# Optimization experiments

Measured on AMD Instinct MI355X. Metric: run time of the kernel, lower is better.

## Reference

```python
import jax, jax.numpy as jnp
import numpy as np

N, E, G = 50000, 800000, 64
IN, HID, H, C, OUT = 4, 128, 2, 64, 7  # HID = heads*C = 128
EPS = 1e-5
NEG_SLOPE = 0.2


def setup_inputs() -> dict:
    key = jax.random.key(0)
    ks = jax.random.split(key, 24)
    rn = lambda k, shape, s=0.1: (jax.random.normal(k, shape, jnp.float32) * s)
    inp = {
        "x": jax.random.normal(ks[0], (N, IN), jnp.float32),
        "edge_index": jax.random.randint(ks[1], (2, E), 0, N, jnp.int64),
        "batch": jnp.sort(jax.random.randint(ks[2], (N,), 0, G, jnp.int64)),
        # GATv2 layer 1: lin_l (source), lin_r (target), attention vector, bias
        "Wl1": rn(ks[3], (IN, HID)), "Wr1": rn(ks[4], (IN, HID)),
        "att1": rn(ks[5], (H, C)), "b1": rn(ks[6], (HID,)),
        "g1": jnp.ones((HID,), jnp.float32), "be1": jnp.zeros((HID,), jnp.float32),
        # GATv2 layer 2
        "Wl2": rn(ks[7], (HID, HID)), "Wr2": rn(ks[8], (HID, HID)),
        "att2": rn(ks[9], (H, C)), "b2": rn(ks[10], (HID,)),
        "g2": jnp.ones((HID,), jnp.float32), "be2": jnp.zeros((HID,), jnp.float32),
        # MLP head
        "W3": rn(ks[11], (HID, C)), "b3": rn(ks[12], (C,)),
        "W4": rn(ks[13], (C, OUT)), "b4": rn(ks[14], (OUT,)),
    }
    return inp


def gatv2_conv(x, src, dst, Wl, Wr, att, bias):
    """PyG GATv2Conv, heads=H, concat=True, self-loops already in (src,dst)."""
    n = x.shape[0]
    xl = (x @ Wl).reshape(n, H, C)  # source-side transform
    xr = (x @ Wr).reshape(n, H, C)  # target-side transform
    m = xl[src] + xr[dst]                                   # [E', H, C]
    e = jnp.einsum('ehc,hc->eh', jax.nn.leaky_relu(m, NEG_SLOPE), att)
    # segment softmax over edges sharing a destination node
    emax = jax.ops.segment_max(e, dst, num_segments=n)
    p = jnp.exp(e - emax[dst])
    denom = jax.ops.segment_sum(p, dst, num_segments=n)
    alpha = p / denom[dst]                                  # [E', H]
    out = jax.ops.segment_sum(alpha[..., None] * xl[src], dst, num_segments=n)
    return out.reshape(n, H * C) + bias


def batchnorm(x, gamma, beta):
    mu = jnp.mean(x, axis=0)
    var = jnp.mean(jnp.square(x - mu), axis=0)  # biased var (torch train norm)
    return gamma * (x - mu) * jax.lax.rsqrt(var + EPS) + beta


def reference(x, edge_index, batch, Wl1, Wr1, att1, b1, g1, be1,
              Wl2, Wr2, att2, b2, g2, be2, W3, b3, W4, b4):
    n = x.shape[0]
    loops = jnp.arange(n, dtype=edge_index.dtype)
    src = jnp.concatenate([edge_index[0], loops])
    dst = jnp.concatenate([edge_index[1], loops])

    h = jax.nn.relu(batchnorm(gatv2_conv(x, src, dst, Wl1, Wr1, att1, b1), g1, be1))
    h = jax.nn.relu(batchnorm(gatv2_conv(h, src, dst, Wl2, Wr2, att2, b2), g2, be2))

    # global mean pool over graphs
    sums = jax.ops.segment_sum(h, batch, num_segments=G)
    cnts = jax.ops.segment_sum(jnp.ones((n, 1), h.dtype), batch, num_segments=G)
    pooled = sums / jnp.maximum(cnts, 1.0)

    out = jax.nn.relu(pooled @ W3 + b3)
    return out @ W4 + b4
```

## Files before the change

kernel.cpp:

```cpp
#include <hip/hip_runtime.h>
#include <hip/hip_bf16.h>

typedef __hip_bfloat16 bf16;
typedef unsigned short u16;
typedef unsigned int u32;
typedef long long i64;
typedef short bf16x8 __attribute__((ext_vector_type(8)));
typedef float f32x4 __attribute__((ext_vector_type(4)));

#define N_NODES 50000
#define E_EDGES 800000
#define G_GRAPHS 64
#define HID 128
#define OUT_F 7
#define EPSBN 1e-5f
#define NEG 0.2f
#define NB_G 2048
#define SCAN_B 196
#define PB_NODES 32
#define XP 136
#define NXF 25000
#define NEB 3125
#define NB_X 1024
#define NTILES 3125

__device__ __forceinline__ float b2f(bf16 v) { return __bfloat162float(v); }
__device__ __forceinline__ float ldf(const void* p, int i, int fm) {
    return fm ? ((const float*)p)[i] : b2f(((const bf16*)p)[i]);
}
__device__ __forceinline__ int ldi(const void* p, i64 i, int im) {
    return im ? (int)((const i64*)p)[i] : ((const int*)p)[i];
}
__device__ __forceinline__ void stf(void* p, int i, int fm, float v) {
    if (fm) ((float*)p)[i] = v; else ((bf16*)p)[i] = __float2bfloat16(v);
}
__device__ __forceinline__ float bl(u32 u) { return __uint_as_float(u << 16); }
__device__ __forceinline__ float bh(u32 u) { return __uint_as_float(u & 0xFFFF0000u); }

template <int CTRL>
__device__ __forceinline__ float dpp_add(float t) {
    int v = __builtin_amdgcn_update_dpp(0, __float_as_int(t), CTRL, 0xF, 0xF, true);
    return t + __int_as_float(v);
}

__global__ void k_init(const void* __restrict__ x, const void* __restrict__ ei,
                       int* __restrict__ flags,
                       float* __restrict__ z1, int n1, float* __restrict__ z2, int n2) {
    int t = threadIdx.x;
    if (blockIdx.x == 0) {
        __shared__ int sh[2];
        if (t == 0) { sh[0] = 0; sh[1] = 1; }
        __syncthreads();
        const u16* xb = (const u16*)x;
        int huge = 0;
        for (int i = t; i < 1024; i += 256) {
            int e = (xb[i] >> 7) & 0xFF;
            if (e >= 0x90) huge = 1;
        }
        if (huge) atomicOr(&sh[0], 1);
        const u32* eb = (const u32*)ei;
        int nz = 0;
        for (int i = t; i < 512; i += 256)
            if (eb[2 * i + 1] != 0) nz = 1;
        if (nz) atomicAnd(&sh[1], 0);
        __syncthreads();
        if (t == 0) { flags[0] = sh[0]; flags[1] = sh[1]; }
    } else {
        int i = (blockIdx.x - 1) * 256 + t;
        int stride = (gridDim.x - 1) * 256;
        for (; i < n1 + n2; i += stride) {
            if (i < n1) z1[i] = 0.0f;
            else z2[i - n1] = 0.0f;
        }
    }
}

__global__ void k_deg(const void* __restrict__ ei, const int* __restrict__ flags,
                      int* __restrict__ deg) {
    int im = flags[1];
    int e = blockIdx.x * 256 + threadIdx.x;
    if (e >= E_EDGES) return;
    int d = ldi(ei, (i64)E_EDGES + e, im);
    atomicAdd(&deg[d], 1);
}

__global__ void k_scan1(const int* __restrict__ deg, int* __restrict__ bsum) {
    __shared__ int s[256];
    int t = threadIdx.x, i = blockIdx.x * 256 + t;
    s[t] = (i < N_NODES) ? deg[i] : 0;
    __syncthreads();
    for (int off = 128; off > 0; off >>= 1) {
        if (t < off) s[t] += s[t + off];
        __syncthreads();
    }
    if (t == 0) bsum[blockIdx.x] = s[0];
}

__global__ void k_scan2(int* __restrict__ bsum) {
    __shared__ int s[256];
    int t = threadIdx.x;
    int orig = (t < SCAN_B) ? bsum[t] : 0;
    s[t] = orig;
    __syncthreads();
    for (int off = 1; off < 256; off <<= 1) {
        int v = (t >= off) ? s[t - off] : 0;
        __syncthreads();
        s[t] += v;
        __syncthreads();
    }
    if (t < SCAN_B) bsum[t] = s[t] - orig;
}

__global__ void k_scan3(const int* __restrict__ deg, const int* __restrict__ bsum,
                        int* __restrict__ rowptr, int* __restrict__ cursor) {
    __shared__ int s[256];
    int t = threadIdx.x, i = blockIdx.x * 256 + t;
    int v = (i < N_NODES) ? deg[i] : 0;
    s[t] = v;
    __syncthreads();
    for (int off = 1; off < 256; off <<= 1) {
        int a = (t >= off) ? s[t - off] : 0;
        __syncthreads();
        s[t] += a;
        __syncthreads();
    }
    int excl = s[t] - v + bsum[blockIdx.x];
    if (i < N_NODES) { rowptr[i] = excl; cursor[i] = excl; }
    if (i == N_NODES - 1) rowptr[N_NODES] = excl + v;
}

__global__ __launch_bounds__(256) void k_fillprep(
    const void* __restrict__ ei, int* __restrict__ cursor, u16* __restrict__ csr,
    const void* __restrict__ x, const void* __restrict__ Wl, const void* __restrict__ Wr,
    const void* __restrict__ Wl2, const void* __restrict__ Wr2,
    const int* __restrict__ flags,
    bf16* __restrict__ xl, bf16* __restrict__ xr, bf16* __restrict__ WT) {
    int b = blockIdx.x;
    if (b < NEB) {
        int im = flags[1];
        int e = b * 256 + threadIdx.x;
        if (e < E_EDGES) {
            int src = ldi(ei, e, im);
            int d   = ldi(ei, (i64)E_EDGES + e, im);
            int pos = atomicAdd(&cursor[d], 1);
            csr[pos] = (u16)src;
        }
    } else if (b < NEB + NXF) {
        int fm = flags[0];
        int idx = (b - NEB) * 256 + threadIdx.x;
        int n = idx >> 7, j = idx & 127;
        float a = 0.f, bb = 0.f;
#pragma unroll
        for (int k = 0; k < 4; k++) {
            float xv = ldf(x, n * 4 + k, fm);
            a += xv * ldf(Wl, k * HID + j, fm);
            bb += xv * ldf(Wr, k * HID + j, fm);
        }
        xl[idx] = __float2bfloat16(a);
        xr[idx] = __float2bfloat16(bb);
    } else {
        int fm = flags[0];
        int idx = (b - NEB - NXF) * 256 + threadIdx.x;
        int mat = idx >> 14, r = idx & 16383, j = r >> 7, k = r & 127;
        const void* W = mat ? Wr2 : Wl2;
        WT[idx] = __float2bfloat16(ldf(W, k * HID + j, fm));
    }
}

__global__ __launch_bounds__(256) void k_gather(
    const bf16* __restrict__ XLp, const bf16* __restrict__ XRp,
    const void* __restrict__ att, const void* __restrict__ bias,
    const int* __restrict__ rowptr, const u16* __restrict__ csr,
    const int* __restrict__ flags,
    float* __restrict__ A, float* __restrict__ partial) {
    __shared__ float ls[128], lq[128];
    int t = threadIdx.x;
    if (t < 128) { ls[t] = 0.f; lq[t] = 0.f; }
    __syncthreads();
    int fm = flags[0];
    int lane = t & 63, waveid = t >> 6;
    int half = lane >> 5;
    int headq = (lane >> 4) & 1;
    int c16 = lane & 15;
    int cbase = headq * 64 + c16 * 4;
    const u32* XLw = (const u32*)XLp;
    const u32* XRw = (const u32*)XRp;
    u32 coff = (u32)(cbase >> 1);
    float a0 = ldf(att, cbase + 0, fm), a1 = ldf(att, cbase + 1, fm);
    float a2 = ldf(att, cbase + 2, fm), a3 = ldf(att, cbase + 3, fm);
    float bb0 = ldf(bias, cbase + 0, fm), bb1 = ldf(bias, cbase + 1, fm);
    float bb2 = ldf(bias, cbase + 2, fm), bb3 = ldf(bias, cbase + 3, fm);
    float s0 = 0, s1 = 0, s2 = 0, s3 = 0, q0 = 0, q1 = 0, q2 = 0, q3 = 0;

    for (int d = blockIdx.x * 4 + waveid; d < N_NODES; d += NB_G * 4) {
        int rp = rowptr[d];
        int deg = rowptr[d + 1] - rp;
        int count = deg + 1;
        u32 roff = ((u32)d << 6) + coff;
        u32 r01 = XRw[roff], r23 = XRw[roff + 1];
        float xr0 = bl(r01), xr1 = bh(r01), xr2 = bl(r23), xr3 = bh(r23);
        float acc0 = 0, acc1 = 0, acc2 = 0, acc3 = 0, den = 0;
        int sA = d; if (half < deg) sA = (int)csr[rp + half];
        int sB = d; if (2 + half < deg) sB = (int)csr[rp + 2 + half];
        u32 offA = ((u32)sA << 6) + coff;
        u32 a01 = XLw[offA], a23 = XLw[offA + 1];
        u32 offB = ((u32)sB << 6) + coff;
        u32 b01 = XLw[offB], b23 = XLw[offB + 1];
        int sC = d; if (4 + half < deg) sC = (int)csr[rp + 4 + half];
        int sD = d; if (6 + half < deg) sD = (int)csr[rp + 6 + half];
        for (int i = 0; i < count; i += 4) {
            u32 offC = ((u32)sC << 6) + coff;
            u32 n01 = XLw[offC], n23 = XLw[offC + 1];
            u32 offD = ((u32)sD << 6) + coff;
            u32 m01 = XLw[offD], m23 = XLw[offD + 1];
            int eE = i + 8 + half, eF = i + 10 + half;
            int sE = d; if (eE < deg) sE = (int)csr[rp + eE];
            int sF = d; if (eF < deg) sF = (int)csr[rp + eF];
            {
                float x0 = bl(a01), x1 = bh(a01), x2 = bl(a23), x3 = bh(a23);
                float m0 = x0 + xr0, m1 = x1 + xr1, m2 = x2 + xr2, m3 = x3 + xr3;
                m0 = fmaxf(m0, NEG * m0);
                m1 = fmaxf(m1, NEG * m1);
                m2 = fmaxf(m2, NEG * m2);
                m3 = fmaxf(m3, NEG * m3);
                float tt = fmaf(m0, a0, fmaf(m1, a1, fmaf(m2, a2, m3 * a3)));
                tt = dpp_add<0xB1>(tt);
                tt = dpp_add<0x4E>(tt);
                tt = dpp_add<0x141>(tt);
                tt = dpp_add<0x140>(tt);
                float p = __expf(tt);
                if (i + half >= count) p = 0.f;
                den += p;
                acc0 = fmaf(p, x0, acc0); acc1 = fmaf(p, x1, acc1);
                acc2 = fmaf(p, x2, acc2); acc3 = fmaf(p, x3, acc3);
            }
            {
                float x0 = bl(b01), x1 = bh(b01), x2 = bl(b23), x3 = bh(b23);
                float m0 = x0 + xr0, m1 = x1 + xr1, m2 = x2 + xr2, m3 = x3 + xr3;
                m0 = fmaxf(m0, NEG * m0);
                m1 = fmaxf(m1, NEG * m1);
                m2 = fmaxf(m2, NEG * m2);
                m3 = fmaxf(m3, NEG * m3);
                float tt = fmaf(m0, a0, fmaf(m1, a1, fmaf(m2, a2, m3 * a3)));
                tt = dpp_add<0xB1>(tt);
                tt = dpp_add<0x4E>(tt);
                tt = dpp_add<0x141>(tt);
                tt = dpp_add<0x140>(tt);
                float p = __expf(tt);
                if (i + 2 + half >= count) p = 0.f;
                den += p;
                acc0 = fmaf(p, x0, acc0); acc1 = fmaf(p, x1, acc1);
                acc2 = fmaf(p, x2, acc2); acc3 = fmaf(p, x3, acc3);
            }
            a01 = n01; a23 = n23; b01 = m01; b23 = m23;
            sC = sE; sD = sF;
        }
        acc0 += __shfl_xor(acc0, 32, 64);
        acc1 += __shfl_xor(acc1, 32, 64);
        acc2 += __shfl_xor(acc2, 32, 64);
        acc3 += __shfl_xor(acc3, 32, 64);
        den  += __shfl_xor(den, 32, 64);
        if (lane < 32) {
            float inv = __builtin_amdgcn_rcpf(den);
            float v0 = fmaf(acc0, inv, bb0);
            float v1 = fmaf(acc1, inv, bb1);
            float v2 = fmaf(acc2, inv, bb2);
            float v3 = fmaf(acc3, inv, bb3);
            *(float4*)(A + (size_t)d * HID + cbase) = make_float4(v0, v1, v2, v3);
            s0 += v0; s1 += v1; s2 += v2; s3 += v3;
            q0 += v0 * v0; q1 += v1 * v1; q2 += v2 * v2; q3 += v3 * v3;
        }
    }
    if (lane < 32) {
        atomicAdd(&ls[cbase + 0], s0); atomicAdd(&ls[cbase + 1], s1);
        atomicAdd(&ls[cbase + 2], s2); atomicAdd(&ls[cbase + 3], s3);
        atomicAdd(&lq[cbase + 0], q0); atomicAdd(&lq[cbase + 1], q1);
        atomicAdd(&lq[cbase + 2], q2); atomicAdd(&lq[cbase + 3], q3);
    }
    __syncthreads();
    if (t < 128) partial[blockIdx.x * 256 + t] = ls[t];
    else if (t < 256) partial[blockIdx.x * 256 + t] = lq[t - 128];
}

__global__ __launch_bounds__(256) void k_bnred(const float* __restrict__ partial,
                                               float* __restrict__ sums) {
    int t = threadIdx.x;
    float acc = 0.f;
    for (int b = blockIdx.x; b < NB_G; b += 256) acc += partial[b * 256 + t];
    unsafeAtomicAdd(&sums[t], acc);
}

__device__ __forceinline__ void bn_params_lds(
    const float* __restrict__ sums, const void* __restrict__ g, const void* __restrict__ be,
    int fm, float* scs, float* shs, int t) {
    if (t < 128) {
        float mu = sums[t] * (1.0f / N_NODES);
        float var = sums[t + 128] * (1.0f / N_NODES) - mu * mu;
        float sc = ldf(g, t, fm) * rsqrtf(var + EPSBN);
        scs[t] = sc;
        shs[t] = ldf(be, t, fm) - mu * sc;
    }
}

__global__ __launch_bounds__(256) void k_xform2(
    const float* __restrict__ A, const float* __restrict__ sums,
    const void* __restrict__ g, const void* __restrict__ be,
    const int* __restrict__ flags,
    const bf16* __restrict__ WT, bf16* __restrict__ XLp, bf16* __restrict__ XRp) {
    __shared__ __align__(16) bf16 at[16 * XP];
    __shared__ float scs[128], shs[128];
    int t = threadIdx.x;
    int fm = flags[0];
    bn_params_lds(sums, g, be, fm, scs, shs, t);
    int lane = t & 63, w = t >> 6;
    int mat = w & 1, half = w >> 1;
    bf16* outp = mat ? XRp : XLp;
    int l15 = lane & 15, quad = lane >> 4;
    bf16x8 bfrag[4][4];
    {
        const bf16* wbase = WT + mat * HID * HID;
#pragma unroll
        for (int nt = 0; nt < 4; nt++)
#pragma unroll
            for (int ks = 0; ks < 4; ks++)
                bfrag[nt][ks] = *(const bf16x8*)(
                    wbase + ((half * 4 + nt) * 16 + l15) * HID + ks * 32 + quad * 8);
    }
    __syncthreads();
    int sn = t >> 4, sc = (t & 15) * 8;
    for (int tile = blockIdx.x; tile < NTILES; tile += NB_X) {
        int n0 = tile * 16;
        {
            const float4* src = (const float4*)(A + (size_t)(n0 + sn) * HID + sc);
            float4 f0 = src[0], f1 = src[1];
            float v[8] = {f0.x, f0.y, f0.z, f0.w, f1.x, f1.y, f1.z, f1.w};
            u32 pk[4];
#pragma unroll
            for (int i = 0; i < 8; i++) {
                float vv = fmaf(v[i], scs[sc + i], shs[sc + i]);
                v[i] = vv > 0.f ? vv : 0.f;
            }
#pragma unroll
            for (int i = 0; i < 4; i++) {
                u32 lo = __bfloat16_as_ushort(__float2bfloat16(v[2 * i]));
                u32 hi = __bfloat16_as_ushort(__float2bfloat16(v[2 * i + 1]));
                pk[i] = lo | (hi << 16);
            }
            u32* dst = (u32*)(at + sn * XP + sc);
            dst[0] = pk[0]; dst[1] = pk[1]; dst[2] = pk[2]; dst[3] = pk[3];
        }
        __syncthreads();
        f32x4 acc[4] = {{0,0,0,0},{0,0,0,0},{0,0,0,0},{0,0,0,0}};
#pragma unroll
        for (int ks = 0; ks < 4; ks++) {
            bf16x8 af = *(const bf16x8*)(at + l15 * XP + ks * 32 + quad * 8);
#pragma unroll
            for (int nt = 0; nt < 4; nt++)
                acc[nt] = __builtin_amdgcn_mfma_f32_16x16x32_bf16(af, bfrag[nt][ks], acc[nt], 0, 0, 0);
        }
#pragma unroll
        for (int nt = 0; nt < 4; nt++) {
            int j = half * 64 + nt * 16 + l15;
#pragma unroll
            for (int r = 0; r < 4; r++) {
                int n = n0 + quad * 4 + r;
                outp[(size_t)n * HID + j] = __float2bfloat16(acc[nt][r]);
            }
        }
        __syncthreads();
    }
}

__global__ __launch_bounds__(256) void k_pool(
    const float* __restrict__ A, const float* __restrict__ sums,
    const void* __restrict__ g, const void* __restrict__ be,
    const void* __restrict__ batch, const int* __restrict__ flags,
    float* __restrict__ pools, float* __restrict__ cnt) {
    __shared__ float scs[128], shs[128];
    int t = threadIdx.x;
    int fm = flags[0], im = flags[1];
    bn_params_lds(sums, g, be, fm, scs, shs, t);
    __syncthreads();
    int j = t & 127, sub = t >> 7;
    int nstart = blockIdx.x * PB_NODES + sub;
    int nend = min(blockIdx.x * PB_NODES + PB_NODES, N_NODES);
    float sc = scs[j], sh = shs[j];
    float acc = 0.f; int run = 0; int gcur = -1;
    for (int n = nstart; n < nend; n += 2) {
        int gg = ldi(batch, n, im);
        if (gg != gcur) {
            if (run > 0) {
                unsafeAtomicAdd(&pools[gcur * HID + j], acc);
                if (j == 0) unsafeAtomicAdd(&cnt[gcur], (float)run);
            }
            gcur = gg; acc = 0.f; run = 0;
        }
        float v = fmaf(A[(size_t)n * HID + j], sc, sh);
        acc += v > 0.f ? v : 0.f;
        run++;
    }
    if (run > 0) {
        unsafeAtomicAdd(&pools[gcur * HID + j], acc);
        if (j == 0) unsafeAtomicAdd(&cnt[gcur], (float)run);
    }
}

__global__ __launch_bounds__(64) void k_head(
    const float* __restrict__ pools, const float* __restrict__ cnt,
    const void* __restrict__ W3, const void* __restrict__ b3,
    const void* __restrict__ W4, const void* __restrict__ b4,
    const int* __restrict__ flags, void* __restrict__ out) {
    __shared__ float p[HID];
    __shared__ float z[64];
    int fm = flags[0];
    int g = blockIdx.x, t = threadIdx.x;
    float inv = 1.0f / fmaxf(cnt[g], 1.0f);
    p[t]      = pools[g * HID + t] * inv;
    p[t + 64] = pools[g * HID + 64 + t] * inv;
    __syncthreads();
    float acc = ldf(b3, t, fm);
    for (int j = 0; j < HID; j++) acc += p[j] * ldf(W3, j * 64 + t, fm);
    z[t] = acc > 0.f ? acc : 0.f;
    __syncthreads();
    if (t < OUT_F) {
        float o = ldf(b4, t, fm);
        for (int c = 0; c < 64; c++) o += z[c] * ldf(W4, c * OUT_F + t, fm);
        stf(out, g * OUT_F + t, fm, o);
    }
}

extern "C" void kernel_launch(void* const* d_in, const int* in_sizes, int n_in,
                              void* d_out, int out_size, void* d_ws, size_t ws_size,
                              hipStream_t stream) {
    const void* x    = d_in[0];
    const void* ei   = d_in[1];
    const void* batch= d_in[2];
    const void* Wl1  = d_in[3];
    const void* Wr1  = d_in[4];
    const void* att1 = d_in[5];
    const void* b1   = d_in[6];
    const void* g1   = d_in[7];
    const void* be1  = d_in[8];
    const void* Wl2  = d_in[9];
    const void* Wr2  = d_in[10];
    const void* att2 = d_in[11];
    const void* b2   = d_in[12];
    const void* g2   = d_in[13];
    const void* be2  = d_in[14];
    const void* W3   = d_in[15];
    const void* b3   = d_in[16];
    const void* W4   = d_in[17];
    const void* b4   = d_in[18];

    int*   flags  = (int*)d_ws;
    float* A      = (float*)((char*)d_ws + 64);
    int*   deg    = (int*)A;
    int*   rowptr = (int*)(A + (size_t)N_NODES * HID);
    u16*   csr    = (u16*)(rowptr + (N_NODES + 1));
    float* partial= (float*)(csr + E_EDGES);
    int*   cursor = (int*)partial;
    float* pools  = partial + (size_t)NB_G * 256;
    float* cnt    = pools + G_GRAPHS * HID;
    float* bnS1   = cnt + G_GRAPHS;
    float* bnS2   = bnS1 + 256;
    int*   bsum   = (int*)(bnS2 + 256);
    bf16*  WT     = (bf16*)(bsum + 256);
    bf16*  XL     = WT + 2 * HID * HID;
    bf16*  XR     = XL + (size_t)N_NODES * HID;

    const size_t NEEDED = 64
        + sizeof(float) * (size_t)N_NODES * HID
        + sizeof(int) * ((size_t)N_NODES + 1)
        + sizeof(u16) * (size_t)E_EDGES
        + sizeof(float) * ((size_t)NB_G * 256 + G_GRAPHS * HID + G_GRAPHS + 512 + 256)
        + sizeof(bf16) * (2 * HID * HID + 2 * (size_t)N_NODES * HID);
    if (ws_size < NEEDED) return;

    const int zlen2 = G_GRAPHS * HID + G_GRAPHS + 512;

    k_init<<<129, 256, 0, stream>>>(x, ei, flags, (float*)deg, N_NODES, pools, zlen2);
    k_deg<<<NEB, 256, 0, stream>>>(ei, flags, deg);

    k_scan1<<<SCAN_B, 256, 0, stream>>>(deg, bsum);
    k_scan2<<<1, 256, 0, stream>>>(bsum);
    k_scan3<<<SCAN_B, 256, 0, stream>>>(deg, bsum, rowptr, cursor);

    k_fillprep<<<NEB + NXF + 128, 256, 0, stream>>>(
        ei, cursor, csr, x, Wl1, Wr1, Wl2, Wr2, flags, XL, XR, WT);

    k_gather<<<NB_G, 256, 0, stream>>>(XL, XR, att1, b1, rowptr, csr, flags, A, partial);
    k_bnred<<<256, 256, 0, stream>>>(partial, bnS1);

    k_xform2<<<NB_X, 256, 0, stream>>>(A, bnS1, g1, be1, flags, WT, XL, XR);
    k_gather<<<NB_G, 256, 0, stream>>>(XL, XR, att2, b2, rowptr, csr, flags, A, partial);
    k_bnred<<<256, 256, 0, stream>>>(partial, bnS2);

    k_pool<<<(N_NODES + PB_NODES - 1) / PB_NODES, 256, 0, stream>>>(
        A, bnS2, g2, be2, batch, flags, pools, cnt);
    k_head<<<G_GRAPHS, 64, 0, stream>>>(pools, cnt, W3, b3, W4, b4, flags, d_out);
}
```

Measured before the change: 370.3 us.

## Build CSR via bucketed binning instead of degree count plus global scan

```diff
diff --git a/kernel.cpp b/kernel.cpp
--- a/kernel.cpp
+++ b/kernel.cpp
@@ -16,13 +16,14 @@
 #define EPSBN 1e-5f
 #define NEG 0.2f
 #define NB_G 2048
-#define SCAN_B 196
 #define PB_NODES 32
 #define XP 136
 #define NXF 25000
 #define NEB 3125
 #define NB_X 1024
 #define NTILES 3125
+#define NBUCK 196
+#define BCAP 4608
 
 __device__ __forceinline__ float b2f(bf16 v) { return __bfloat162float(v); }
 __device__ __forceinline__ float ldf(const void* p, int i, int fm) {
@@ -44,8 +45,7 @@
 }
 
 __global__ void k_init(const void* __restrict__ x, const void* __restrict__ ei,
-                       int* __restrict__ flags,
-                       float* __restrict__ z1, int n1, float* __restrict__ z2, int n2) {
+                       int* __restrict__ flags, float* __restrict__ z1, int n1) {
     int t = threadIdx.x;
     if (blockIdx.x == 0) {
         __shared__ int sh[2];
@@ -68,69 +68,12 @@
     } else {
         int i = (blockIdx.x - 1) * 256 + t;
         int stride = (gridDim.x - 1) * 256;
-        for (; i < n1 + n2; i += stride) {
-            if (i < n1) z1[i] = 0.0f;
-            else z2[i - n1] = 0.0f;
-        }
-    }
-}
-
-__global__ void k_deg(const void* __restrict__ ei, const int* __restrict__ flags,
-                      int* __restrict__ deg) {
-    int im = flags[1];
-    int e = blockIdx.x * 256 + threadIdx.x;
-    if (e >= E_EDGES) return;
-    int d = ldi(ei, (i64)E_EDGES + e, im);
-    atomicAdd(&deg[d], 1);
-}
-
-__global__ void k_scan1(const int* __restrict__ deg, int* __restrict__ bsum) {
-    __shared__ int s[256];
-    int t = threadIdx.x, i = blockIdx.x * 256 + t;
-    s[t] = (i < N_NODES) ? deg[i] : 0;
-    __syncthreads();
-    for (int off = 128; off > 0; off >>= 1) {
-        if (t < off) s[t] += s[t + off];
-        __syncthreads();
-    }
-    if (t == 0) bsum[blockIdx.x] = s[0];
-}
-
-__global__ void k_scan2(int* __restrict__ bsum) {
-    __shared__ int s[256];
-    int t = threadIdx.x;
-    int orig = (t < SCAN_B) ? bsum[t] : 0;
-    s[t] = orig;
-    __syncthreads();
-    for (int off = 1; off < 256; off <<= 1) {
-        int v = (t >= off) ? s[t - off] : 0;
-        __syncthreads();
-        s[t] += v;
-        __syncthreads();
-    }
-    if (t < SCAN_B) bsum[t] = s[t] - orig;
-}
-
-__global__ void k_scan3(const int* __restrict__ deg, const int* __restrict__ bsum,
-                        int* __restrict__ rowptr, int* __restrict__ cursor) {
-    __shared__ int s[256];
-    int t = threadIdx.x, i = blockIdx.x * 256 + t;
-    int v = (i < N_NODES) ? deg[i] : 0;
-    s[t] = v;
-    __syncthreads();
-    for (int off = 1; off < 256; off <<= 1) {
-        int a = (t >= off) ? s[t - off] : 0;
-        __syncthreads();
-        s[t] += a;
-        __syncthreads();
-    }
-    int excl = s[t] - v + bsum[blockIdx.x];
-    if (i < N_NODES) { rowptr[i] = excl; cursor[i] = excl; }
-    if (i == N_NODES - 1) rowptr[N_NODES] = excl + v;
-}
-
-__global__ __launch_bounds__(256) void k_fillprep(
-    const void* __restrict__ ei, int* __restrict__ cursor, u16* __restrict__ csr,
+        for (; i < n1; i += stride) z1[i] = 0.0f;
+    }
+}
+
+__global__ __launch_bounds__(256) void k_binprep(
+    const void* __restrict__ ei, int* __restrict__ counters, u32* __restrict__ bbuf,
     const void* __restrict__ x, const void* __restrict__ Wl, const void* __restrict__ Wr,
     const void* __restrict__ Wl2, const void* __restrict__ Wr2,
     const int* __restrict__ flags,
@@ -142,8 +85,9 @@
         if (e < E_EDGES) {
             int src = ldi(ei, e, im);
             int d   = ldi(ei, (i64)E_EDGES + e, im);
-            int pos = atomicAdd(&cursor[d], 1);
-            csr[pos] = (u16)src;
+            int bucket = d >> 8, dl = d & 255;
+            int pos = atomicAdd(&counters[bucket * 16], 1);
+            if (pos < BCAP) bbuf[bucket * BCAP + pos] = (u32)src | ((u32)dl << 16);
         }
     } else if (b < NEB + NXF) {
         int fm = flags[0];
@@ -164,6 +108,46 @@
         int mat = idx >> 14, r = idx & 16383, j = r >> 7, k = r & 127;
         const void* W = mat ? Wr2 : Wl2;
         WT[idx] = __float2bfloat16(ldf(W, k * HID + j, fm));
+    }
+}
+
+__global__ __launch_bounds__(256) void k_build(
+    const int* __restrict__ counters, const u32* __restrict__ bbuf,
+    int* __restrict__ rowptr, u16* __restrict__ csr) {
+    __shared__ int scnt[256], ldeg[256], lrow[256], lcur[256];
+    int t = threadIdx.x, b = blockIdx.x;
+    int cntb = min(counters[b * 16], BCAP);
+    scnt[t] = (t < NBUCK) ? min(counters[t * 16], BCAP) : 0;
+    __syncthreads();
+    for (int off = 1; off < 256; off <<= 1) {
+        int v = (t >= off) ? scnt[t - off] : 0;
+        __syncthreads();
+        scnt[t] += v;
+        __syncthreads();
+    }
+    int base_b = (b == 0) ? 0 : scnt[b - 1];
+    ldeg[t] = 0;
+    __syncthreads();
+    for (int i = t; i < cntb; i += 256)
+        atomicAdd(&ldeg[bbuf[b * BCAP + i] >> 16], 1);
+    __syncthreads();
+    lrow[t] = ldeg[t];
+    __syncthreads();
+    for (int off = 1; off < 256; off <<= 1) {
+        int v = (t >= off) ? lrow[t - off] : 0;
+        __syncthreads();
+        lrow[t] += v;
+        __syncthreads();
+    }
+    int excl = lrow[t] - ldeg[t];
+    int node = b * 256 + t;
+    if (node <= N_NODES) rowptr[node] = base_b + excl;
+    lcur[t] = excl;
+    __syncthreads();
+    for (int i = t; i < cntb; i += 256) {
+        u32 v = bbuf[b * BCAP + i];
+        int pos = atomicAdd(&lcur[v >> 16], 1);
+        csr[base_b + pos] = (u16)(v & 0xFFFF);
     }
 }
 
@@ -454,17 +438,16 @@
 
     int*   flags  = (int*)d_ws;
     float* A      = (float*)((char*)d_ws + 64);
-    int*   deg    = (int*)A;
     int*   rowptr = (int*)(A + (size_t)N_NODES * HID);
     u16*   csr    = (u16*)(rowptr + (N_NODES + 1));
-    float* partial= (float*)(csr + E_EDGES);
-    int*   cursor = (int*)partial;
+    u32*   bbuf   = (u32*)(csr + E_EDGES);
+    float* partial= (float*)(bbuf + (size_t)NBUCK * BCAP);
     float* pools  = partial + (size_t)NB_G * 256;
     float* cnt    = pools + G_GRAPHS * HID;
     float* bnS1   = cnt + G_GRAPHS;
     float* bnS2   = bnS1 + 256;
-    int*   bsum   = (int*)(bnS2 + 256);
-    bf16*  WT     = (bf16*)(bsum + 256);
+    int*   counters = (int*)(bnS2 + 256);
+    bf16*  WT     = (bf16*)(counters + NBUCK * 16);
     bf16*  XL     = WT + 2 * HID * HID;
     bf16*  XR     = XL + (size_t)N_NODES * HID;
 
@@ -472,21 +455,18 @@
         + sizeof(float) * (size_t)N_NODES * HID
         + sizeof(int) * ((size_t)N_NODES + 1)
         + sizeof(u16) * (size_t)E_EDGES
-        + sizeof(float) * ((size_t)NB_G * 256 + G_GRAPHS * HID + G_GRAPHS + 512 + 256)
+        + sizeof(u32) * (size_t)NBUCK * BCAP
+        + sizeof(float) * ((size_t)NB_G * 256 + G_GRAPHS * HID + G_GRAPHS + 512)
+        + sizeof(int) * NBUCK * 16
         + sizeof(bf16) * (2 * HID * HID + 2 * (size_t)N_NODES * HID);
     if (ws_size < NEEDED) return;
 
-    const int zlen2 = G_GRAPHS * HID + G_GRAPHS + 512;
-
-    k_init<<<129, 256, 0, stream>>>(x, ei, flags, (float*)deg, N_NODES, pools, zlen2);
-    k_deg<<<NEB, 256, 0, stream>>>(ei, flags, deg);
-
-    k_scan1<<<SCAN_B, 256, 0, stream>>>(deg, bsum);
-    k_scan2<<<1, 256, 0, stream>>>(bsum);
-    k_scan3<<<SCAN_B, 256, 0, stream>>>(deg, bsum, rowptr, cursor);
-
-    k_fillprep<<<NEB + NXF + 128, 256, 0, stream>>>(
-        ei, cursor, csr, x, Wl1, Wr1, Wl2, Wr2, flags, XL, XR, WT);
+    const int zlen = G_GRAPHS * HID + G_GRAPHS + 512 + NBUCK * 16;
+
+    k_init<<<129, 256, 0, stream>>>(x, ei, flags, pools, zlen);
+    k_binprep<<<NEB + NXF + 128, 256, 0, stream>>>(
+        ei, counters, bbuf, x, Wl1, Wr1, Wl2, Wr2, flags, XL, XR, WT);
+    k_build<<<NBUCK, 256, 0, stream>>>(counters, bbuf, rowptr, csr);
 
     k_gather<<<NB_G, 256, 0, stream>>>(XL, XR, att1, b1, rowptr, csr, flags, A, partial);
     k_bnred<<<256, 256, 0, stream>>>(partial, bnS1);
```

New measurement: 384.2 us. 3.7% more time.
